# Kernel optimization log

Hardware: AMD Instinct MI355X
Metric: run time of the kernel (lower is better)

## Reference

```python
import jax, jax.numpy as jnp
import numpy as np

DIM = 512
HEADS = 16
HEAD_DIM = DIM // HEADS
SCALE = HEAD_DIM ** -0.5


def setup_inputs() -> dict:
    key = jax.random.key(0)
    k = jax.random.split(key, 6)
    B_, N = 2048, 49
    nW = 64
    x = jax.random.normal(k[0], (B_, N, DIM), dtype=jnp.float32)
    mask = jax.random.normal(k[1], (nW, N, N), dtype=jnp.float32)
    W_qkv = jax.random.normal(k[2], (3 * DIM, DIM), dtype=jnp.float32) * 0.02
    b_qkv = jnp.zeros((3 * DIM,), dtype=jnp.float32)
    W_proj = jax.random.normal(k[3], (DIM, DIM), dtype=jnp.float32) * 0.02
    b_proj = jnp.zeros((DIM,), dtype=jnp.float32)
    return {"x": x, "mask": mask, "W_qkv": W_qkv, "b_qkv": b_qkv,
            "W_proj": W_proj, "b_proj": b_proj}


def reference(x, mask, W_qkv, b_qkv, W_proj, b_proj):
    B_, N, C = x.shape
    H, d = HEADS, HEAD_DIM
    nW = mask.shape[0]
    # qkv projection: [B_, N, 3, H, d] -> q,k,v each [B_, H, N, d]
    qkv = (x @ W_qkv.T + b_qkv).reshape(B_, N, 3, H, d)
    qkv = jnp.transpose(qkv, (2, 0, 3, 1, 4))
    q, k, v = qkv[0], qkv[1], qkv[2]
    attn = jnp.einsum('bhnd,bhmd->bhnm', q * SCALE, k)  # [B_, H, N, N]
    # add per-window additive mask, broadcast over B_//nW groups and heads
    attn = attn.reshape(B_ // nW, nW, H, N, N) + mask[None, :, None, :, :]
    attn = attn.reshape(B_, H, N, N)
    attn = jax.nn.softmax(attn, axis=-1)
    out = jnp.einsum('bhnm,bhmd->bhnd', attn, v)  # [B_, H, N, d]
    out = jnp.transpose(out, (0, 2, 1, 3)).reshape(B_, N, C)
    return out @ W_proj.T + b_proj
```

## Files before the change

kernel.cpp:

```cpp
#include <hip/hip_runtime.h>


typedef unsigned short ushort_t;
typedef __bf16 bf16x8 __attribute__((ext_vector_type(8)));
typedef float f32x4 __attribute__((ext_vector_type(4)));
typedef unsigned short us8 __attribute__((ext_vector_type(8)));

#define SCALE_F 0.17677669529663687f

__device__ __forceinline__ ushort_t f2bf(float f) {
  unsigned u = __builtin_bit_cast(unsigned, f);
  u += 0x7FFFu + ((u >> 16) & 1u);
  return (ushort_t)(u >> 16);
}

__device__ __forceinline__ void gload_lds16(const void* g, void* l) {
  __builtin_amdgcn_global_load_lds(
      (const __attribute__((address_space(1))) void*)g,
      (__attribute__((address_space(3))) void*)l, 16, 0, 0);
}

__device__ __forceinline__ void lds_fence() {
  asm volatile("s_waitcnt lgkmcnt(0)" ::: "memory");
}

__device__ __forceinline__ int swzkey(int r) {
  return ((r >> 2) & 3) ^ ((r >> 1) & 1);
}

__global__ __launch_bounds__(256) void k_cvt(const float* __restrict__ in,
                                             ushort_t* __restrict__ out, int n4) {
  int i = blockIdx.x * blockDim.x + threadIdx.x;
  if (i >= n4) return;
  float4 v = reinterpret_cast<const float4*>(in)[i];
  ushort4 o = make_ushort4(f2bf(v.x), f2bf(v.y), f2bf(v.z), f2bf(v.w));
  reinterpret_cast<ushort4*>(out)[i] = o;
}

__global__ __launch_bounds__(256) void k_cvtwq(const float* __restrict__ in,
                                               ushort_t* __restrict__ out, int n4) {
  int i = blockIdx.x * blockDim.x + threadIdx.x;
  if (i >= n4) return;
  const float sc = (i < (262144 / 4)) ? SCALE_F : 1.0f;
  float4 v = reinterpret_cast<const float4*>(in)[i];
  ushort4 o = make_ushort4(f2bf(v.x * sc), f2bf(v.y * sc),
                           f2bf(v.z * sc), f2bf(v.w * sc));
  reinterpret_cast<ushort4*>(out)[i] = o;
}

__global__ __launch_bounds__(256) void k_bs(const float* __restrict__ b,
                                            float* __restrict__ bs) {
  int i = blockIdx.x * blockDim.x + threadIdx.x;
  if (i < 1536) bs[i] = b[i] * (i < 512 ? SCALE_F : 1.0f);
}

__global__ __launch_bounds__(256) void k_maskx(const float* __restrict__ mask,
                                               float* __restrict__ maskx) {
  const int i = blockIdx.x * blockDim.x + threadIdx.x;
  const int ni = i & 3, arow = (i >> 2) & 15, qr = (i >> 6) & 63, w = i >> 12;
  const int col = ni * 16 + arow;
  float v = -100.0f;
  if (qr < 49 && col < 49) v = mask[((size_t)w * 49 + qr) * 49 + col];
  maskx[i] = v;
}

template <int EPI>
__global__ __launch_bounds__(256) void k_gemm(const ushort_t* __restrict__ A,
                                              const ushort_t* __restrict__ W,
                                              const float* __restrict__ bias,
                                              ushort_t* __restrict__ out_qkv,
                                              float* __restrict__ out_f,
                                              int nt_o) {
  __shared__ __align__(16) ushort_t As[128][32];
  __shared__ __align__(16) ushort_t Ws[128][32];

  const int tid  = threadIdx.x;
  const int lane = tid & 63;
  const int wv   = tid >> 6;
  const int wr   = wv >> 1, wc = wv & 1;

  const int cpx = gridDim.x >> 3;
  const int lid = (blockIdx.x & 7) * cpx + (blockIdx.x >> 3);
  const int bm  = lid / nt_o;
  const int bo  = lid - bm * nt_o;
  const size_t m0 = (size_t)bm * 128;
  const int o0    = bo * 128;

  f32x4 acc[4][4];
#pragma unroll
  for (int i = 0; i < 4; i++)
#pragma unroll
    for (int j = 0; j < 4; j++) acc[i][j] = f32x4{0.f, 0.f, 0.f, 0.f};

  const int srow = lane >> 2;
  const int scol = ((lane & 3) ^ swzkey(srow)) * 8;

  for (int kt = 0; kt < 16; ++kt) {
    const int k0 = kt * 32;
#pragma unroll
    for (int i = 0; i < 2; i++) {
      const int rb = i * 64 + wv * 16;
      gload_lds16(A + (m0 + rb + srow) * 512 + k0 + scol, &As[rb][0]);
    }
#pragma unroll
    for (int i = 0; i < 2; i++) {
      const int rb = i * 64 + wv * 16;
      gload_lds16(W + (size_t)(o0 + rb + srow) * 512 + k0 + scol, &Ws[rb][0]);
    }
    __syncthreads();
    const int fr = lane & 15;
    const int cb = ((lane >> 4) ^ swzkey(fr)) << 3;
    uint4 ar[4], br[4];
#pragma unroll
    for (int mi = 0; mi < 4; mi++)
      ar[mi] = *reinterpret_cast<const uint4*>(&As[wr * 64 + mi * 16 + fr][cb]);
#pragma unroll
    for (int ni = 0; ni < 4; ni++)
      br[ni] = *reinterpret_cast<const uint4*>(&Ws[wc * 64 + ni * 16 + fr][cb]);
#pragma unroll
    for (int mi = 0; mi < 4; mi++)
#pragma unroll
      for (int ni = 0; ni < 4; ni++)
        acc[mi][ni] = __builtin_amdgcn_mfma_f32_16x16x32_bf16(
            __builtin_bit_cast(bf16x8, ar[mi]),
            __builtin_bit_cast(bf16x8, br[ni]), acc[mi][ni], 0, 0, 0);
    __syncthreads();
  }

  const int colbase = lane & 15;
  const int rowgrp  = (lane >> 4) * 4;

  if constexpr (EPI == 1) {
#pragma unroll
    for (int ni = 0; ni < 4; ni++) {
      const int o = o0 + wc * 64 + ni * 16 + colbase;
      const float bv = bias[o];
#pragma unroll
      for (int mi = 0; mi < 4; mi++) {
        const size_t mrow = m0 + wr * 64 + mi * 16 + rowgrp;
#pragma unroll
        for (int r = 0; r < 4; r++)
          out_f[(mrow + r) * 512 + o] = acc[mi][ni][r] + bv;
      }
    }
  } else {
#pragma unroll
    for (int mi = 0; mi < 4; mi++) {
#pragma unroll
      for (int r = 0; r < 4; r++) {
        const size_t t = m0 + wr * 64 + mi * 16 + rowgrp + r;
        ushort_t* rowp = out_qkv + t * 1536;
#pragma unroll
        for (int ni = 0; ni < 4; ni++) {
          const int o = o0 + wc * 64 + ni * 16 + colbase;
          rowp[o] = f2bf(acc[mi][ni][r] + bias[o]);
        }
      }
    }
  }
}

__global__ __launch_bounds__(256) void k_attn4(const ushort_t* __restrict__ qkv,
                                               const float* __restrict__ maskx,
                                               ushort_t* __restrict__ aout) {
  __shared__ __align__(16) ushort_t Vt[4][32][64];
  __shared__ __align__(16) ushort_t Ps[4][16][64];

  const int tid  = threadIdx.x;
  const int lane = tid & 63;
  const int wv   = tid >> 6;
  const int blk  = blockIdx.x;
  const int b    = blk >> 2;
  const int h    = (blk & 3) * 4 + wv;
  const int w    = b & 63;
  const size_t tb = (size_t)b * 49 * 1536 + (size_t)h * 32;
  const ushort_t* qb = qkv + tb;
  const ushort_t* kb = qkv + tb + 512;
  const ushort_t* vb = qkv + tb + 1024;

  {
    uint4* vz = reinterpret_cast<uint4*>(&Vt[wv][0][0]);
#pragma unroll
    for (int i = 0; i < 4; i++) vz[i * 64 + lane] = make_uint4(0, 0, 0, 0);
  }
#pragma unroll
  for (int i = 0; i < 4; i++) {
    const int e = lane + (i << 6);
    if (e < 196) {
      const int n = e >> 2, d0 = (e & 3) * 8;
      uint4 raw = *reinterpret_cast<const uint4*>(vb + (size_t)n * 1536 + d0);
      us8 ev = __builtin_bit_cast(us8, raw);
#pragma unroll
      for (int j = 0; j < 8; j++)
        Vt[wv][d0 + j][(((n >> 3) ^ j) << 3) | (n & 7)] = ev[j];
    }
  }
  lds_fence();

  const int arow = lane & 15;
  const int kc   = (lane >> 4) * 8;
  const int rg   = (lane >> 4) * 4;
  const float* mxb = maskx + ((size_t)w * 64 + rg) * 16 * 4 + (size_t)arow * 4;

  uint4 vf0[2], vf1[2];
#pragma unroll
  for (int kk = 0; kk < 2; kk++) {
    const int ch = kk * 4 + (lane >> 4);
    const int cb = ((ch ^ (lane & 7)) << 3);
    vf0[kk] = *reinterpret_cast<const uint4*>(&Vt[wv][arow][cb]);
    vf1[kk] = *reinterpret_cast<const uint4*>(&Vt[wv][16 + arow][cb]);
  }

  uint4 kf[4];
#pragma unroll
  for (int ni = 0; ni < 4; ni++)
    kf[ni] = *reinterpret_cast<const uint4*>(kb + (size_t)(ni * 16 + arow) * 1536 + kc);

  bf16x8 ones;
#pragma unroll
  for (int i = 0; i < 8; i++) ones[i] = (__bf16)1.0f;

#pragma unroll
  for (int mt = 0; mt < 4; mt++) {
    {
      uint4 qraw = *reinterpret_cast<const uint4*>(qb + (size_t)(mt * 16 + arow) * 1536 + kc);
      bf16x8 qa = __builtin_bit_cast(bf16x8, qraw);
      f32x4 s[4];
#pragma unroll
      for (int ni = 0; ni < 4; ni++) {
        f32x4 z = {0.f, 0.f, 0.f, 0.f};
        s[ni] = __builtin_amdgcn_mfma_f32_16x16x32_bf16(
            qa, __builtin_bit_cast(bf16x8, kf[ni]), z, 0, 0, 0);
      }
#pragma unroll
      for (int r = 0; r < 4; r++) {
        const int prow = rg + r;
        f32x4 mv = *reinterpret_cast<const f32x4*>(mxb + ((size_t)mt * 16 + r) * 64);
#pragma unroll
        for (int ni = 0; ni < 4; ni++) {
          const float p = __expf(s[ni][r] + mv[ni]);
          const int pcol = ni * 16 + arow;
          Ps[wv][prow][(((pcol >> 3) ^ (prow & 7)) << 3) | (pcol & 7)] = f2bf(p);
        }
      }
    }
    lds_fence();

    {
      f32x4 o0 = {0.f, 0.f, 0.f, 0.f}, o1 = {0.f, 0.f, 0.f, 0.f};
      f32x4 o2 = {0.f, 0.f, 0.f, 0.f};
#pragma unroll
      for (int kk = 0; kk < 2; kk++) {
        const int ch = kk * 4 + (lane >> 4);
        const int cb = ((ch ^ (lane & 7)) << 3);
        uint4 praw = *reinterpret_cast<const uint4*>(&Ps[wv][arow][cb]);
        bf16x8 pa = __builtin_bit_cast(bf16x8, praw);
        o0 = __builtin_amdgcn_mfma_f32_16x16x32_bf16(
            pa, __builtin_bit_cast(bf16x8, vf0[kk]), o0, 0, 0, 0);
        o1 = __builtin_amdgcn_mfma_f32_16x16x32_bf16(
            pa, __builtin_bit_cast(bf16x8, vf1[kk]), o1, 0, 0, 0);
        o2 = __builtin_amdgcn_mfma_f32_16x16x32_bf16(pa, ones, o2, 0, 0, 0);
      }
#pragma unroll
      for (int r = 0; r < 4; r++) {
        const int qr = mt * 16 + rg + r;
        if (qr < 49) {
          const float inv = 1.f / o2[r];
          aout[((size_t)b * 49 + qr) * 512 + h * 32 + arow]      = f2bf(o0[r] * inv);
          aout[((size_t)b * 49 + qr) * 512 + h * 32 + 16 + arow] = f2bf(o1[r] * inv);
        }
      }
    }
    lds_fence();
  }
}

extern "C" void kernel_launch(void* const* d_in, const int* in_sizes, int n_in,
                              void* d_out, int out_size, void* d_ws, size_t ws_size,
                              hipStream_t stream) {
  const float* x      = (const float*)d_in[0];
  const float* mask   = (const float*)d_in[1];
  const float* W_qkv  = (const float*)d_in[2];
  const float* b_qkv  = (const float*)d_in[3];
  const float* W_proj = (const float*)d_in[4];
  const float* b_proj = (const float*)d_in[5];
  float* out = (float*)d_out;

  ushort_t* ws     = (ushort_t*)d_ws;
  ushort_t* xb     = ws;
  ushort_t* qkvb   = ws + 51380224UL;
  ushort_t* aoutb  = ws + 205520896UL;
  ushort_t* wqkvb  = ws + 256901120UL;
  ushort_t* wprojb = ws + 257687552UL;
  float*    maskxb = (float*)(ws + 257949696UL);
  float*    bscale = (float*)(ws + 258473984UL);

  const int n4x = 51380224 / 4, n4q = 786432 / 4, n4p = 262144 / 4;
  k_cvt<<<(n4x + 255) / 256, 256, 0, stream>>>(x, xb, n4x);
  k_cvtwq<<<(n4q + 255) / 256, 256, 0, stream>>>(W_qkv, wqkvb, n4q);
  k_cvt<<<(n4p + 255) / 256, 256, 0, stream>>>(W_proj, wprojb, n4p);
  k_bs<<<6, 256, 0, stream>>>(b_qkv, bscale);
  k_maskx<<<262144 / 256, 256, 0, stream>>>(mask, maskxb);

  k_gemm<0><<<784 * 12, 256, 0, stream>>>(xb, wqkvb, bscale, qkvb, nullptr, 12);

  k_attn4<<<2048 * 4, 256, 0, stream>>>(qkvb, maskxb, aoutb);

  k_gemm<1><<<784 * 4, 256, 0, stream>>>(aoutb, wprojb, b_proj, nullptr, out, 4);
}
```

Before: 570.0 us.

## Load GEMM MFMA operands directly from global memory, dropping LDS staging

```diff
diff --git a/kernel.cpp b/kernel.cpp
--- a/kernel.cpp
+++ b/kernel.cpp
@@ -14,18 +14,8 @@
   return (ushort_t)(u >> 16);
 }
 
-__device__ __forceinline__ void gload_lds16(const void* g, void* l) {
-  __builtin_amdgcn_global_load_lds(
-      (const __attribute__((address_space(1))) void*)g,
-      (__attribute__((address_space(3))) void*)l, 16, 0, 0);
-}
-
 __device__ __forceinline__ void lds_fence() {
   asm volatile("s_waitcnt lgkmcnt(0)" ::: "memory");
-}
-
-__device__ __forceinline__ int swzkey(int r) {
-  return ((r >> 2) & 3) ^ ((r >> 1) & 1);
 }
 
 __global__ __launch_bounds__(256) void k_cvt(const float* __restrict__ in,
@@ -65,15 +55,12 @@
 }
 
 template <int EPI>
-__global__ __launch_bounds__(256) void k_gemm(const ushort_t* __restrict__ A,
-                                              const ushort_t* __restrict__ W,
-                                              const float* __restrict__ bias,
-                                              ushort_t* __restrict__ out_qkv,
-                                              float* __restrict__ out_f,
-                                              int nt_o) {
-  __shared__ __align__(16) ushort_t As[128][32];
-  __shared__ __align__(16) ushort_t Ws[128][32];
-
+__global__ __launch_bounds__(256) void k_gemmD(const ushort_t* __restrict__ A,
+                                               const ushort_t* __restrict__ W,
+                                               const float* __restrict__ bias,
+                                               ushort_t* __restrict__ out_qkv,
+                                               float* __restrict__ out_f,
+                                               int nt_o) {
   const int tid  = threadIdx.x;
   const int lane = tid & 63;
   const int wv   = tid >> 6;
@@ -86,45 +73,38 @@
   const size_t m0 = (size_t)bm * 128;
   const int o0    = bo * 128;
 
+  const int fr = lane & 15;
+  const int lq = lane >> 4;
+
+  const ushort_t* Ab = A + (m0 + wr * 64 + fr) * 512 + lq * 8;
+  const ushort_t* Wb = W + (size_t)(o0 + wc * 64 + fr) * 512 + lq * 8;
+
   f32x4 acc[4][4];
 #pragma unroll
   for (int i = 0; i < 4; i++)
 #pragma unroll
     for (int j = 0; j < 4; j++) acc[i][j] = f32x4{0.f, 0.f, 0.f, 0.f};
 
-  const int srow = lane >> 2;
-  const int scol = ((lane & 3) ^ swzkey(srow)) * 8;
-
-  for (int kt = 0; kt < 16; ++kt) {
-    const int k0 = kt * 32;
-#pragma unroll
-    for (int i = 0; i < 2; i++) {
-      const int rb = i * 64 + wv * 16;
-      gload_lds16(A + (m0 + rb + srow) * 512 + k0 + scol, &As[rb][0]);
-    }
-#pragma unroll
-    for (int i = 0; i < 2; i++) {
-      const int rb = i * 64 + wv * 16;
-      gload_lds16(W + (size_t)(o0 + rb + srow) * 512 + k0 + scol, &Ws[rb][0]);
-    }
-    __syncthreads();
-    const int fr = lane & 15;
-    const int cb = ((lane >> 4) ^ swzkey(fr)) << 3;
-    uint4 ar[4], br[4];
-#pragma unroll
-    for (int mi = 0; mi < 4; mi++)
-      ar[mi] = *reinterpret_cast<const uint4*>(&As[wr * 64 + mi * 16 + fr][cb]);
-#pragma unroll
-    for (int ni = 0; ni < 4; ni++)
-      br[ni] = *reinterpret_cast<const uint4*>(&Ws[wc * 64 + ni * 16 + fr][cb]);
-#pragma unroll
-    for (int mi = 0; mi < 4; mi++)
+#pragma unroll 2
+  for (int kt = 0; kt < 8; ++kt) {
+#pragma unroll
+    for (int kk = 0; kk < 2; ++kk) {
+      const int ko = kt * 64 + kk * 32;
+      uint4 ar[4], br[4];
+#pragma unroll
+      for (int mi = 0; mi < 4; mi++)
+        ar[mi] = *reinterpret_cast<const uint4*>(Ab + (size_t)mi * (16 * 512) + ko);
 #pragma unroll
       for (int ni = 0; ni < 4; ni++)
-        acc[mi][ni] = __builtin_amdgcn_mfma_f32_16x16x32_bf16(
-            __builtin_bit_cast(bf16x8, ar[mi]),
-            __builtin_bit_cast(bf16x8, br[ni]), acc[mi][ni], 0, 0, 0);
-    __syncthreads();
+        br[ni] = *reinterpret_cast<const uint4*>(Wb + (size_t)ni * (16 * 512) + ko);
+#pragma unroll
+      for (int mi = 0; mi < 4; mi++)
+#pragma unroll
+        for (int ni = 0; ni < 4; ni++)
+          acc[mi][ni] = __builtin_amdgcn_mfma_f32_16x16x32_bf16(
+              __builtin_bit_cast(bf16x8, ar[mi]),
+              __builtin_bit_cast(bf16x8, br[ni]), acc[mi][ni], 0, 0, 0);
+    }
   }
 
   const int colbase = lane & 15;
@@ -302,9 +282,9 @@
   k_bs<<<6, 256, 0, stream>>>(b_qkv, bscale);
   k_maskx<<<262144 / 256, 256, 0, stream>>>(mask, maskxb);
 
-  k_gemm<0><<<784 * 12, 256, 0, stream>>>(xb, wqkvb, bscale, qkvb, nullptr, 12);
+  k_gemmD<0><<<784 * 12, 256, 0, stream>>>(xb, wqkvb, bscale, qkvb, nullptr, 12);
 
   k_attn4<<<2048 * 4, 256, 0, stream>>>(qkvb, maskxb, aoutb);
 
-  k_gemm<1><<<784 * 4, 256, 0, stream>>>(aoutb, wprojb, b_proj, nullptr, out, 4);
-}
+  k_gemmD<1><<<784 * 4, 256, 0, stream>>>(aoutb, wprojb, b_proj, nullptr, out, 4);
+}
```

Result: slower. 979.5 us (+71.8%).
